# Kernel tuning notes

Hardware: AMD Instinct MI355X
Metric: run time of the kernel (lower is better)

Reference implementation:

```python
import jax, jax.numpy as jnp
import numpy as np

N = 100000
E = 1600000
IN_C, HID_C, OUT_C = 512, 128, 40
K = 5
ALPHA = 0.5


def setup_inputs() -> dict:
    key = jax.random.key(0)
    k1, k2, k3, k4, k5, k6 = jax.random.split(key, 6)
    x = jax.random.normal(k1, (N, IN_C), dtype=jnp.float32)
    edge_index = jax.random.randint(k2, (2, E), 0, N, dtype=jnp.int64)
    # lin1: in -> hidden, lin2: hidden -> out (Kaiming-uniform-ish scale)
    W1 = jax.random.normal(k3, (IN_C, HID_C), dtype=jnp.float32) * (1.0 / np.sqrt(IN_C))
    b1 = jax.random.normal(k4, (HID_C,), dtype=jnp.float32) * 0.01
    W2 = jax.random.normal(k5, (HID_C, OUT_C), dtype=jnp.float32) * (1.0 / np.sqrt(HID_C))
    b2 = jax.random.normal(k6, (OUT_C,), dtype=jnp.float32) * 0.01
    return {"x": x, "edge_index": edge_index, "W1": W1, "b1": b1, "W2": W2, "b2": b2}


def _gcn_norm(edge_index, num_nodes):
    # add self-loops with weight 1, then symmetric normalization D^-1/2 A D^-1/2
    loops = jnp.arange(num_nodes, dtype=edge_index.dtype)
    row = jnp.concatenate([edge_index[0], loops])
    col = jnp.concatenate([edge_index[1], loops])
    w = jnp.ones(row.shape[0], dtype=jnp.float32)
    deg = jax.ops.segment_sum(w, col, num_segments=num_nodes)
    dinv = jnp.where(deg > 0, jax.lax.rsqrt(deg), 0.0)
    norm = dinv[row] * w * dinv[col]
    return row, col, norm


def reference(x, edge_index, W1, b1, W2, b2):
    h = x @ W1 + b1                      # [N, HID_C]
    row, col, norm = _gcn_norm(edge_index, N)
    x0 = h
    for _ in range(K):
        # gather source features, scale by edge norm, scatter-add to targets
        agg = jax.ops.segment_sum(norm[:, None] * h[row], col, num_segments=N)
        h = (1.0 - ALPHA) * agg + ALPHA * x0
    return h @ W2 + b2                   # [N, OUT_C]
```

## Files before the change

### kernel.cpp

```cpp
#include <hip/hip_runtime.h>
#include <hip/hip_bf16.h>

#define NN 100000
#define EE 1600000
#define HALFN 50000

typedef __attribute__((ext_vector_type(8))) short short8;
typedef __attribute__((ext_vector_type(4))) float f32x4;

__device__ __forceinline__ unsigned short f2bfu(float f) {
    __hip_bfloat16 h = __float2bfloat16(f);
    return *reinterpret_cast<unsigned short*>(&h);
}
__device__ __forceinline__ float bf2f(unsigned short u) {
    return __uint_as_float((unsigned int)u << 16);
}


__global__ void wct_kernel(const float* __restrict__ W1, const float* __restrict__ W2,
                           const float* __restrict__ b1, short* __restrict__ WcT,
                           float* __restrict__ bc) {
    int t = blockIdx.x * 256 + threadIdx.x;
    if (t < 48 * 512) {
        int j = t >> 9, k = t & 511;
        float s = 0.f;
        if (j < 40)
            for (int i = 0; i < 128; ++i) s = fmaf(W1[k * 128 + i], W2[i * 40 + j], s);
        WcT[j * 512 + k] = (short)f2bfu(s);
    } else if (t < 48 * 512 + 48) {
        int j = t - 48 * 512;
        float s = 0.f;
        if (j < 40)
            for (int i = 0; i < 128; ++i) s = fmaf(b1[i], W2[i * 40 + j], s);
        bc[j] = s;
    }
}

__global__ __launch_bounds__(256) void gemm_z0(const float* __restrict__ x,
                                               const short* __restrict__ WcT,
                                               const float* __restrict__ bc,
                                               unsigned short* __restrict__ z0) {
    const int tid = threadIdx.x;
    const int lane = tid & 63;
    const int wave = tid >> 6;
    const int rbase = blockIdx.x * 64 + wave * 16;
    const int row = rbase + (lane & 15);
    const int kc = lane >> 4;
    const bool rok = row < NN;

    f32x4 acc0 = {0.f, 0.f, 0.f, 0.f};
    f32x4 acc1 = {0.f, 0.f, 0.f, 0.f};
    f32x4 acc2 = {0.f, 0.f, 0.f, 0.f};

    const float* xrow = x + (size_t)row * 512 + kc * 8;
    const short* bp0 = WcT + (size_t)(lane & 15) * 512 + kc * 8;
    const short* bp1 = bp0 + 16 * 512;
    const short* bp2 = bp0 + 32 * 512;

    for (int k0 = 0; k0 < 512; k0 += 32) {
        float4 p0 = {0.f, 0.f, 0.f, 0.f}, p1 = {0.f, 0.f, 0.f, 0.f};
        if (rok) {
            p0 = *reinterpret_cast<const float4*>(xrow + k0);
            p1 = *reinterpret_cast<const float4*>(xrow + k0 + 4);
        }
        short8 a;
        a[0] = (short)f2bfu(p0.x); a[1] = (short)f2bfu(p0.y);
        a[2] = (short)f2bfu(p0.z); a[3] = (short)f2bfu(p0.w);
        a[4] = (short)f2bfu(p1.x); a[5] = (short)f2bfu(p1.y);
        a[6] = (short)f2bfu(p1.z); a[7] = (short)f2bfu(p1.w);
        short8 b0 = *reinterpret_cast<const short8*>(bp0 + k0);
        short8 b1 = *reinterpret_cast<const short8*>(bp1 + k0);
        short8 b2 = *reinterpret_cast<const short8*>(bp2 + k0);
        acc0 = __builtin_amdgcn_mfma_f32_16x16x32_bf16(a, b0, acc0, 0, 0, 0);
        acc1 = __builtin_amdgcn_mfma_f32_16x16x32_bf16(a, b1, acc1, 0, 0, 0);
        acc2 = __builtin_amdgcn_mfma_f32_16x16x32_bf16(a, b2, acc2, 0, 0, 0);
    }

    const int cb = lane & 15;
    const int rr = rbase + (lane >> 4) * 4;
#pragma unroll
    for (int q = 0; q < 4; ++q) {
        int r = rr + q;
        if (r < NN) {
            z0[(size_t)r * 64 + cb] = f2bfu(acc0[q] + bc[cb]);
            z0[(size_t)r * 64 + cb + 16] = f2bfu(acc1[q] + bc[cb + 16]);
            z0[(size_t)r * 64 + cb + 32] = f2bfu(acc2[q] + bc[cb + 32]);
            z0[(size_t)r * 64 + cb + 48] = 0;
        }
    }
}

__global__ void count_kernel(const int* __restrict__ eidx, int* __restrict__ counts) {
    int e = blockIdx.x * 256 + threadIdx.x;
    if (e < EE) atomicAdd(&counts[eidx[EE + e]], 1);
}

__global__ void scan1(const int* __restrict__ counts, int* __restrict__ ptr,
                      int* __restrict__ bsum) {
    __shared__ int s[256];
    int tid = threadIdx.x;
    int i = blockIdx.x * 256 + tid;
    int v = (i < NN) ? counts[i] : 0;
    s[tid] = v;
    __syncthreads();
    for (int off = 1; off < 256; off <<= 1) {
        int t = (tid >= off) ? s[tid - off] : 0;
        __syncthreads();
        s[tid] += t;
        __syncthreads();
    }
    if (i < NN) ptr[i] = s[tid] - v;
    if (tid == 255) bsum[blockIdx.x] = s[255];
}

__global__ void scan2(int* __restrict__ bsum) {
    __shared__ int s[512];
    int tid = threadIdx.x;
    int v = (tid < 391) ? bsum[tid] : 0;
    s[tid] = v;
    __syncthreads();
    for (int off = 1; off < 512; off <<= 1) {
        int t = (tid >= off) ? s[tid - off] : 0;
        __syncthreads();
        s[tid] += t;
        __syncthreads();
    }
    if (tid < 391) bsum[tid] = s[tid] - v;
}

__global__ void scan3(int* __restrict__ ptr, const int* __restrict__ bsum,
                      const int* __restrict__ counts, float* __restrict__ dinvp,
                      int* __restrict__ ptr2) {
    int i = blockIdx.x * 256 + threadIdx.x;
    if (i < NN) {
        int p = ptr[i] + bsum[blockIdx.x];
        ptr[i] = p;
        ptr2[i] = p;
        dinvp[i] = rsqrtf(1.0f + (float)counts[i]);
    }
    if (i == 0) { ptr[NN] = EE; ptr2[NN] = EE; }
}

__global__ void scatter_kernel(const int* __restrict__ eidx,
                               const float* __restrict__ dinvp, int* __restrict__ ptr2,
                               int2* __restrict__ cev) {
    int e = blockIdx.x * 256 + threadIdx.x;
    if (e < EE) {
        int r = eidx[e];
        int c = eidx[EE + e];
        int pos = atomicAdd(&ptr2[c], 1);
        cev[pos] = make_int2(r, __float_as_int(dinvp[r]));
    }
}

__global__ __launch_bounds__(256, 8) void propagate(const unsigned short* __restrict__ zcur,
                                                    const unsigned short* __restrict__ z0q,
                                                    unsigned short* __restrict__ znb,
                                                    float* __restrict__ outf,
                                                    const int* __restrict__ ptr,
                                                    const int2* __restrict__ cev,
                                                    const float* __restrict__ dinvp,
                                                    const float* __restrict__ b2, int last) {
    const int lane = threadIdx.x & 63;
    const int wid = blockIdx.x * 4 + (threadIdx.x >> 6);
    const int n0 = wid, n1 = wid + HALFN;

    int beg0 = __builtin_amdgcn_readfirstlane(ptr[n0]);
    int end0 = __builtin_amdgcn_readfirstlane(ptr[n0 + 1]);
    int beg1 = __builtin_amdgcn_readfirstlane(ptr[n1]);
    int end1 = __builtin_amdgcn_readfirstlane(ptr[n1 + 1]);
    const float dc0 = dinvp[n0], dc1 = dinvp[n1];

    int m0 = end0 - beg0; if (m0 > 64) m0 = 64;
    int m1 = end1 - beg1; if (m1 > 64) m1 = 64;

    int idx0 = beg0 + (lane < m0 ? lane : m0 - 1); if (idx0 < 0) idx0 = 0;
    int idx1 = beg1 + (lane < m1 ? lane : m1 - 1); if (idx1 < 0) idx1 = 0;
    int2 ev0 = cev[idx0];
    int2 ev1 = cev[idx1];
    if (lane >= m0) ev0.y = 0;
    if (lane >= m1) ev1.y = 0;

    const float self0 = bf2f(zcur[(unsigned)(n0 * 64 + lane)]);
    const float self1 = bf2f(zcur[(unsigned)(n1 * 64 + lane)]);
    const float z00 = bf2f(z0q[(unsigned)(n0 * 64 + lane)]);
    const float z01 = bf2f(z0q[(unsigned)(n1 * 64 + lane)]);

    float A0 = dc0 * self0, B0 = 0.f;
    float A1 = dc1 * self1, B1 = 0.f;

    int nc0 = (m0 + 7) >> 3, nc1 = (m1 + 7) >> 3;
    int nc = nc0 > nc1 ? nc0 : nc1;
    for (int c = 0; c < nc; ++c) {
        const int j = c * 8;
        float x[8], y[8];
#pragma unroll
        for (int k = 0; k < 8; ++k) {
            unsigned r0 = (unsigned)__builtin_amdgcn_readlane(ev0.x, j + k);
            unsigned r1 = (unsigned)__builtin_amdgcn_readlane(ev1.x, j + k);
            x[k] = bf2f(zcur[(r0 << 6) + lane]);
            y[k] = bf2f(zcur[(r1 << 6) + lane]);
        }
#pragma unroll
        for (int k = 0; k < 8; ++k) {
            float w = __int_as_float(__builtin_amdgcn_readlane(ev0.y, j + k));
            float u = __int_as_float(__builtin_amdgcn_readlane(ev1.y, j + k));
            if (k & 1) { B0 = fmaf(w, x[k], B0); B1 = fmaf(u, y[k], B1); }
            else       { A0 = fmaf(w, x[k], A0); A1 = fmaf(u, y[k], A1); }
        }
    }

    for (int e = beg0 + 64; e < end0; ++e) {
        int2 ee = cev[e];
        A0 = fmaf(__int_as_float(ee.y), bf2f(zcur[((unsigned)ee.x << 6) + lane]), A0);
    }
    for (int e = beg1 + 64; e < end1; ++e) {
        int2 ee = cev[e];
        A1 = fmaf(__int_as_float(ee.y), bf2f(zcur[((unsigned)ee.x << 6) + lane]), A1);
    }

    float res0 = 0.5f * dc0 * (A0 + B0) + 0.5f * z00;
    float res1 = 0.5f * dc1 * (A1 + B1) + 0.5f * z01;
    if (last) {
        if (lane < 40) {
            outf[(unsigned)(n0 * 40 + lane)] = res0 + b2[lane];
            outf[(unsigned)(n1 * 40 + lane)] = res1 + b2[lane];
        }
    } else {
        znb[(unsigned)(n0 * 64 + lane)] = f2bfu(res0);
        znb[(unsigned)(n1 * 64 + lane)] = f2bfu(res1);
    }
}

extern "C" void kernel_launch(void* const* d_in, const int* in_sizes, int n_in,
                              void* d_out, int out_size, void* d_ws, size_t ws_size,
                              hipStream_t stream) {
    const float* x  = (const float*)d_in[0];
    const int*   ei = (const int*)d_in[1];
    const float* W1 = (const float*)d_in[2];
    const float* b1 = (const float*)d_in[3];
    const float* W2 = (const float*)d_in[4];
    const float* b2 = (const float*)d_in[5];
    float* out = (float*)d_out;

    char* ws = (char*)d_ws;
    short*          WcT  = (short*)(ws + 0);
    float*          bc   = (float*)(ws + 49152);
    unsigned short* z0   = (unsigned short*)(ws + 65536);
    unsigned short* za   = (unsigned short*)(ws + 12865536);
    unsigned short* zb   = (unsigned short*)(ws + 25665536);
    float*          dinv = (float*)(ws + 38465536);
    int*            cnt  = (int*)(ws + 38865536);
    int*            ptr  = (int*)(ws + 39265536);
    int*            bsum = (int*)(ws + 39665664);
    int*            ptr2 = (int*)(ws + 39667712);
    int2*           cev  = (int2*)(ws + 40067840);

    hipMemsetAsync(cnt, 0, NN * sizeof(int), stream);
    wct_kernel<<<97, 256, 0, stream>>>(W1, W2, b1, WcT, bc);
    count_kernel<<<(EE + 255) / 256, 256, 0, stream>>>(ei, cnt);
    scan1<<<391, 256, 0, stream>>>(cnt, ptr, bsum);
    scan2<<<1, 512, 0, stream>>>(bsum);
    scan3<<<391, 256, 0, stream>>>(ptr, bsum, cnt, dinv, ptr2);
    gemm_z0<<<1563, 256, 0, stream>>>(x, WcT, bc, z0);
    scatter_kernel<<<(EE + 255) / 256, 256, 0, stream>>>(ei, dinv, ptr2, cev);

    propagate<<<12500, 256, 0, stream>>>(z0, z0, zb, out, ptr, cev, dinv, b2, 0);
    propagate<<<12500, 256, 0, stream>>>(zb, z0, za, out, ptr, cev, dinv, b2, 0);
    propagate<<<12500, 256, 0, stream>>>(za, z0, zb, out, ptr, cev, dinv, b2, 0);
    propagate<<<12500, 256, 0, stream>>>(zb, z0, za, out, ptr, cev, dinv, b2, 0);
    propagate<<<12500, 256, 0, stream>>>(za, z0, zb, out, ptr, cev, dinv, b2, 1);
}
```

Measured before the change: 431.0 us.

## Split features into 16-channel planes and propagate each plane separately

```diff
diff --git a/kernel.cpp b/kernel.cpp
--- a/kernel.cpp
+++ b/kernel.cpp
@@ -3,7 +3,7 @@
 
 #define NN 100000
 #define EE 1600000
-#define HALFN 50000
+#define CH_STRIDE 1600000
 
 typedef __attribute__((ext_vector_type(8))) short short8;
 typedef __attribute__((ext_vector_type(4))) float f32x4;
@@ -82,10 +82,10 @@
     for (int q = 0; q < 4; ++q) {
         int r = rr + q;
         if (r < NN) {
-            z0[(size_t)r * 64 + cb] = f2bfu(acc0[q] + bc[cb]);
-            z0[(size_t)r * 64 + cb + 16] = f2bfu(acc1[q] + bc[cb + 16]);
-            z0[(size_t)r * 64 + cb + 32] = f2bfu(acc2[q] + bc[cb + 32]);
-            z0[(size_t)r * 64 + cb + 48] = 0;
+            unsigned ro = ((unsigned)r << 4) + cb;
+            z0[ro] = f2bfu(acc0[q] + bc[cb]);
+            z0[CH_STRIDE + ro] = f2bfu(acc1[q] + bc[cb + 16]);
+            z0[2 * CH_STRIDE + ro] = f2bfu(acc2[q] + bc[cb + 32]);
         }
     }
 }
@@ -153,82 +153,69 @@
     }
 }
 
-__global__ __launch_bounds__(256, 8) void propagate(const unsigned short* __restrict__ zcur,
-                                                    const unsigned short* __restrict__ z0q,
-                                                    unsigned short* __restrict__ znb,
-                                                    float* __restrict__ outf,
-                                                    const int* __restrict__ ptr,
-                                                    const int2* __restrict__ cev,
-                                                    const float* __restrict__ dinvp,
-                                                    const float* __restrict__ b2, int last) {
+__global__ __launch_bounds__(256) void propagate(const unsigned short* __restrict__ zcur,
+                                                 const unsigned short* __restrict__ z0q,
+                                                 unsigned short* __restrict__ znb,
+                                                 float* __restrict__ outf,
+                                                 const int* __restrict__ ptr,
+                                                 const int2* __restrict__ cev,
+                                                 const float* __restrict__ dinvp,
+                                                 const float* __restrict__ b2,
+                                                 int cid, int last) {
     const int lane = threadIdx.x & 63;
+    const int f = lane & 15;
+    const int g = lane >> 4;
     const int wid = blockIdx.x * 4 + (threadIdx.x >> 6);
-    const int n0 = wid, n1 = wid + HALFN;
-
-    int beg0 = __builtin_amdgcn_readfirstlane(ptr[n0]);
-    int end0 = __builtin_amdgcn_readfirstlane(ptr[n0 + 1]);
-    int beg1 = __builtin_amdgcn_readfirstlane(ptr[n1]);
-    int end1 = __builtin_amdgcn_readfirstlane(ptr[n1 + 1]);
-    const float dc0 = dinvp[n0], dc1 = dinvp[n1];
-
-    int m0 = end0 - beg0; if (m0 > 64) m0 = 64;
-    int m1 = end1 - beg1; if (m1 > 64) m1 = 64;
-
-    int idx0 = beg0 + (lane < m0 ? lane : m0 - 1); if (idx0 < 0) idx0 = 0;
-    int idx1 = beg1 + (lane < m1 ? lane : m1 - 1); if (idx1 < 0) idx1 = 0;
-    int2 ev0 = cev[idx0];
-    int2 ev1 = cev[idx1];
-    if (lane >= m0) ev0.y = 0;
-    if (lane >= m1) ev1.y = 0;
-
-    const float self0 = bf2f(zcur[(unsigned)(n0 * 64 + lane)]);
-    const float self1 = bf2f(zcur[(unsigned)(n1 * 64 + lane)]);
-    const float z00 = bf2f(z0q[(unsigned)(n0 * 64 + lane)]);
-    const float z01 = bf2f(z0q[(unsigned)(n1 * 64 + lane)]);
-
-    float A0 = dc0 * self0, B0 = 0.f;
-    float A1 = dc1 * self1, B1 = 0.f;
-
-    int nc0 = (m0 + 7) >> 3, nc1 = (m1 + 7) >> 3;
-    int nc = nc0 > nc1 ? nc0 : nc1;
-    for (int c = 0; c < nc; ++c) {
-        const int j = c * 8;
-        float x[8], y[8];
-#pragma unroll
-        for (int k = 0; k < 8; ++k) {
-            unsigned r0 = (unsigned)__builtin_amdgcn_readlane(ev0.x, j + k);
-            unsigned r1 = (unsigned)__builtin_amdgcn_readlane(ev1.x, j + k);
-            x[k] = bf2f(zcur[(r0 << 6) + lane]);
-            y[k] = bf2f(zcur[(r1 << 6) + lane]);
+    const int n = (wid << 2) + g;
+
+    const int beg = ptr[n];
+    const int deg = ptr[n + 1] - beg;
+    const float dc = dinvp[n];
+    const unsigned roff = ((unsigned)n << 4) + f;
+
+    float acc = dc * bf2f(zcur[roff]);
+    const float z0v = bf2f(z0q[roff]);
+
+    int maxd = deg;
+    maxd = max(maxd, __shfl_xor(maxd, 16, 64));
+    maxd = max(maxd, __shfl_xor(maxd, 32, 64));
+
+    for (int s = 0; s < maxd; s += 4) {
+        int i0, i1, i2, i3;
+        {
+            int t0 = (s + 0 < deg) ? s + 0 : deg - 1;
+            int t1 = (s + 1 < deg) ? s + 1 : deg - 1;
+            int t2 = (s + 2 < deg) ? s + 2 : deg - 1;
+            int t3 = (s + 3 < deg) ? s + 3 : deg - 1;
+            i0 = beg + t0; i0 = i0 < 0 ? 0 : (i0 >= EE ? EE - 1 : i0);
+            i1 = beg + t1; i1 = i1 < 0 ? 0 : (i1 >= EE ? EE - 1 : i1);
+            i2 = beg + t2; i2 = i2 < 0 ? 0 : (i2 >= EE ? EE - 1 : i2);
+            i3 = beg + t3; i3 = i3 < 0 ? 0 : (i3 >= EE ? EE - 1 : i3);
         }
-#pragma unroll
-        for (int k = 0; k < 8; ++k) {
-            float w = __int_as_float(__builtin_amdgcn_readlane(ev0.y, j + k));
-            float u = __int_as_float(__builtin_amdgcn_readlane(ev1.y, j + k));
-            if (k & 1) { B0 = fmaf(w, x[k], B0); B1 = fmaf(u, y[k], B1); }
-            else       { A0 = fmaf(w, x[k], A0); A1 = fmaf(u, y[k], A1); }
-        }
-    }
-
-    for (int e = beg0 + 64; e < end0; ++e) {
-        int2 ee = cev[e];
-        A0 = fmaf(__int_as_float(ee.y), bf2f(zcur[((unsigned)ee.x << 6) + lane]), A0);
-    }
-    for (int e = beg1 + 64; e < end1; ++e) {
-        int2 ee = cev[e];
-        A1 = fmaf(__int_as_float(ee.y), bf2f(zcur[((unsigned)ee.x << 6) + lane]), A1);
-    }
-
-    float res0 = 0.5f * dc0 * (A0 + B0) + 0.5f * z00;
-    float res1 = 0.5f * dc1 * (A1 + B1) + 0.5f * z01;
+        int2 e0 = cev[i0];
+        int2 e1 = cev[i1];
+        int2 e2 = cev[i2];
+        int2 e3 = cev[i3];
+        float x0 = bf2f(zcur[((unsigned)e0.x << 4) + f]);
+        float x1 = bf2f(zcur[((unsigned)e1.x << 4) + f]);
+        float x2 = bf2f(zcur[((unsigned)e2.x << 4) + f]);
+        float x3 = bf2f(zcur[((unsigned)e3.x << 4) + f]);
+        float w0 = (s + 0 < deg) ? __int_as_float(e0.y) : 0.f;
+        float w1 = (s + 1 < deg) ? __int_as_float(e1.y) : 0.f;
+        float w2 = (s + 2 < deg) ? __int_as_float(e2.y) : 0.f;
+        float w3 = (s + 3 < deg) ? __int_as_float(e3.y) : 0.f;
+        acc = fmaf(w0, x0, acc);
+        acc = fmaf(w1, x1, acc);
+        acc = fmaf(w2, x2, acc);
+        acc = fmaf(w3, x3, acc);
+    }
+
+    float res = 0.5f * dc * acc + 0.5f * z0v;
     if (last) {
-        if (lane < 40) {
-            outf[(unsigned)(n0 * 40 + lane)] = res0 + b2[lane];
-            outf[(unsigned)(n1 * 40 + lane)] = res1 + b2[lane];
-        }
+        int j = cid * 16 + f;
+        if (j < 40) outf[(unsigned)n * 40 + j] = res + b2[j];
     } else {
-        znb[(unsigned)(n0 * 64 + lane)] = f2bfu(res0);
-        znb[(unsigned)(n1 * 64 + lane)] = f2bfu(res1);
+        znb[roff] = f2bfu(res);
     }
 }
 
@@ -247,14 +234,14 @@
     short*          WcT  = (short*)(ws + 0);
     float*          bc   = (float*)(ws + 49152);
     unsigned short* z0   = (unsigned short*)(ws + 65536);
-    unsigned short* za   = (unsigned short*)(ws + 12865536);
-    unsigned short* zb   = (unsigned short*)(ws + 25665536);
-    float*          dinv = (float*)(ws + 38465536);
-    int*            cnt  = (int*)(ws + 38865536);
-    int*            ptr  = (int*)(ws + 39265536);
-    int*            bsum = (int*)(ws + 39665664);
-    int*            ptr2 = (int*)(ws + 39667712);
-    int2*           cev  = (int2*)(ws + 40067840);
+    unsigned short* za   = (unsigned short*)(ws + 9665536);
+    unsigned short* zb   = (unsigned short*)(ws + 19265536);
+    float*          dinv = (float*)(ws + 28865536);
+    int*            cnt  = (int*)(ws + 29265536);
+    int*            ptr  = (int*)(ws + 29665664);
+    int*            bsum = (int*)(ws + 30065792);
+    int*            ptr2 = (int*)(ws + 30067840);
+    int2*           cev  = (int2*)(ws + 30467968);
 
     hipMemsetAsync(cnt, 0, NN * sizeof(int), stream);
     wct_kernel<<<97, 256, 0, stream>>>(W1, W2, b1, WcT, bc);
@@ -265,9 +252,14 @@
     gemm_z0<<<1563, 256, 0, stream>>>(x, WcT, bc, z0);
     scatter_kernel<<<(EE + 255) / 256, 256, 0, stream>>>(ei, dinv, ptr2, cev);
 
-    propagate<<<12500, 256, 0, stream>>>(z0, z0, zb, out, ptr, cev, dinv, b2, 0);
-    propagate<<<12500, 256, 0, stream>>>(zb, z0, za, out, ptr, cev, dinv, b2, 0);
-    propagate<<<12500, 256, 0, stream>>>(za, z0, zb, out, ptr, cev, dinv, b2, 0);
-    propagate<<<12500, 256, 0, stream>>>(zb, z0, za, out, ptr, cev, dinv, b2, 0);
-    propagate<<<12500, 256, 0, stream>>>(za, z0, zb, out, ptr, cev, dinv, b2, 1);
-}
+    for (int c = 0; c < 3; ++c) {
+        const unsigned short* z0c = z0 + (size_t)c * CH_STRIDE;
+        unsigned short* zac = za + (size_t)c * CH_STRIDE;
+        unsigned short* zbc = zb + (size_t)c * CH_STRIDE;
+        propagate<<<6250, 256, 0, stream>>>(z0c, z0c, zbc, out, ptr, cev, dinv, b2, c, 0);
+        propagate<<<6250, 256, 0, stream>>>(zbc, z0c, zac, out, ptr, cev, dinv, b2, c, 0);
+        propagate<<<6250, 256, 0, stream>>>(zac, z0c, zbc, out, ptr, cev, dinv, b2, c, 0);
+        propagate<<<6250, 256, 0, stream>>>(zbc, z0c, zac, out, ptr, cev, dinv, b2, c, 0);
+        propagate<<<6250, 256, 0, stream>>>(zac, z0c, zbc, out, ptr, cev, dinv, b2, c, 1);
+    }
+}
```

Measured after the change: 639.3 us. 48.3% more time.

## Sort nodes by in-degree so each wave processes similarly sized node pairs

Applied to the files above, without the earlier changes.

```diff
diff --git a/kernel.cpp b/kernel.cpp
--- a/kernel.cpp
+++ b/kernel.cpp
@@ -3,7 +3,6 @@
 
 #define NN 100000
 #define EE 1600000
-#define HALFN 50000
 
 typedef __attribute__((ext_vector_type(8))) short short8;
 typedef __attribute__((ext_vector_type(4))) float f32x4;
@@ -141,6 +140,39 @@
     if (i == 0) { ptr[NN] = EE; ptr2[NN] = EE; }
 }
 
+__global__ void hist_kernel(const int* __restrict__ counts, int* __restrict__ hist) {
+    int i = blockIdx.x * 256 + threadIdx.x;
+    if (i < NN) {
+        int b = counts[i]; if (b > 255) b = 255;
+        atomicAdd(&hist[b], 1);
+    }
+}
+
+__global__ void hscan_kernel(int* __restrict__ hist) {
+    __shared__ int s[256];
+    int tid = threadIdx.x;
+    int v = hist[tid];
+    s[tid] = v;
+    __syncthreads();
+    for (int off = 1; off < 256; off <<= 1) {
+        int t = (tid >= off) ? s[tid - off] : 0;
+        __syncthreads();
+        s[tid] += t;
+        __syncthreads();
+    }
+    hist[tid] = s[tid] - v;
+}
+
+__global__ void place_kernel(const int* __restrict__ counts, int* __restrict__ hist,
+                             int* __restrict__ perm) {
+    int i = blockIdx.x * 256 + threadIdx.x;
+    if (i < NN) {
+        int b = counts[i]; if (b > 255) b = 255;
+        int pos = atomicAdd(&hist[b], 1);
+        perm[pos] = i;
+    }
+}
+
 __global__ void scatter_kernel(const int* __restrict__ eidx,
                                const float* __restrict__ dinvp, int* __restrict__ ptr2,
                                int2* __restrict__ cev) {
@@ -160,10 +192,12 @@
                                                     const int* __restrict__ ptr,
                                                     const int2* __restrict__ cev,
                                                     const float* __restrict__ dinvp,
-                                                    const float* __restrict__ b2, int last) {
+                                                    const float* __restrict__ b2,
+                                                    const int* __restrict__ perm, int last) {
     const int lane = threadIdx.x & 63;
     const int wid = blockIdx.x * 4 + (threadIdx.x >> 6);
-    const int n0 = wid, n1 = wid + HALFN;
+    const int n0 = __builtin_amdgcn_readfirstlane(perm[2 * wid]);
+    const int n1 = __builtin_amdgcn_readfirstlane(perm[2 * wid + 1]);
 
     int beg0 = __builtin_amdgcn_readfirstlane(ptr[n0]);
     int end0 = __builtin_amdgcn_readfirstlane(ptr[n0 + 1]);
@@ -255,19 +289,25 @@
     int*            bsum = (int*)(ws + 39665664);
     int*            ptr2 = (int*)(ws + 39667712);
     int2*           cev  = (int2*)(ws + 40067840);
+    int*            perm = (int*)(ws + 52867840);
+    int*            hist = (int*)(ws + 53267840);
 
     hipMemsetAsync(cnt, 0, NN * sizeof(int), stream);
+    hipMemsetAsync(hist, 0, 256 * sizeof(int), stream);
     wct_kernel<<<97, 256, 0, stream>>>(W1, W2, b1, WcT, bc);
     count_kernel<<<(EE + 255) / 256, 256, 0, stream>>>(ei, cnt);
     scan1<<<391, 256, 0, stream>>>(cnt, ptr, bsum);
     scan2<<<1, 512, 0, stream>>>(bsum);
     scan3<<<391, 256, 0, stream>>>(ptr, bsum, cnt, dinv, ptr2);
+    hist_kernel<<<391, 256, 0, stream>>>(cnt, hist);
+    hscan_kernel<<<1, 256, 0, stream>>>(hist);
+    place_kernel<<<391, 256, 0, stream>>>(cnt, hist, perm);
     gemm_z0<<<1563, 256, 0, stream>>>(x, WcT, bc, z0);
     scatter_kernel<<<(EE + 255) / 256, 256, 0, stream>>>(ei, dinv, ptr2, cev);
 
-    propagate<<<12500, 256, 0, stream>>>(z0, z0, zb, out, ptr, cev, dinv, b2, 0);
-    propagate<<<12500, 256, 0, stream>>>(zb, z0, za, out, ptr, cev, dinv, b2, 0);
-    propagate<<<12500, 256, 0, stream>>>(za, z0, zb, out, ptr, cev, dinv, b2, 0);
-    propagate<<<12500, 256, 0, stream>>>(zb, z0, za, out, ptr, cev, dinv, b2, 0);
-    propagate<<<12500, 256, 0, stream>>>(za, z0, zb, out, ptr, cev, dinv, b2, 1);
-}
+    propagate<<<12500, 256, 0, stream>>>(z0, z0, zb, out, ptr, cev, dinv, b2, perm, 0);
+    propagate<<<12500, 256, 0, stream>>>(zb, z0, za, out, ptr, cev, dinv, b2, perm, 0);
+    propagate<<<12500, 256, 0, stream>>>(za, z0, zb, out, ptr, cev, dinv, b2, perm, 0);
+    propagate<<<12500, 256, 0, stream>>>(zb, z0, za, out, ptr, cev, dinv, b2, perm, 0);
+    propagate<<<12500, 256, 0, stream>>>(za, z0, zb, out, ptr, cev, dinv, b2, perm, 1);
+}
```

Result: slower. 960.0 us (+122.8%).

## Propagate pre-scaled features y = dinv*z to drop per-edge weights

Applied to the files above, without the earlier changes.

```diff
diff --git a/kernel.cpp b/kernel.cpp
--- a/kernel.cpp
+++ b/kernel.cpp
@@ -36,10 +36,19 @@
     }
 }
 
+__global__ void padzero_kernel(unsigned short* __restrict__ ya,
+                               unsigned short* __restrict__ yb) {
+    int t = threadIdx.x;
+    if (t < 64) ya[(size_t)NN * 64 + t] = 0;
+    else if (t < 128) yb[(size_t)NN * 64 + (t - 64)] = 0;
+}
+
 __global__ __launch_bounds__(256) void gemm_z0(const float* __restrict__ x,
                                                const short* __restrict__ WcT,
                                                const float* __restrict__ bc,
-                                               unsigned short* __restrict__ z0) {
+                                               const float* __restrict__ dinvp,
+                                               unsigned short* __restrict__ z0,
+                                               unsigned short* __restrict__ y0) {
     const int tid = threadIdx.x;
     const int lane = tid & 63;
     const int wave = tid >> 6;
@@ -82,10 +91,18 @@
     for (int q = 0; q < 4; ++q) {
         int r = rr + q;
         if (r < NN) {
-            z0[(size_t)r * 64 + cb] = f2bfu(acc0[q] + bc[cb]);
-            z0[(size_t)r * 64 + cb + 16] = f2bfu(acc1[q] + bc[cb + 16]);
-            z0[(size_t)r * 64 + cb + 32] = f2bfu(acc2[q] + bc[cb + 32]);
+            float dc = dinvp[r];
+            float v0 = acc0[q] + bc[cb];
+            float v1 = acc1[q] + bc[cb + 16];
+            float v2 = acc2[q] + bc[cb + 32];
+            z0[(size_t)r * 64 + cb] = f2bfu(v0);
+            z0[(size_t)r * 64 + cb + 16] = f2bfu(v1);
+            z0[(size_t)r * 64 + cb + 32] = f2bfu(v2);
             z0[(size_t)r * 64 + cb + 48] = 0;
+            y0[(size_t)r * 64 + cb] = f2bfu(dc * v0);
+            y0[(size_t)r * 64 + cb + 16] = f2bfu(dc * v1);
+            y0[(size_t)r * 64 + cb + 32] = f2bfu(dc * v2);
+            y0[(size_t)r * 64 + cb + 48] = 0;
         }
     }
 }
@@ -141,24 +158,23 @@
     if (i == 0) { ptr[NN] = EE; ptr2[NN] = EE; }
 }
 
-__global__ void scatter_kernel(const int* __restrict__ eidx,
-                               const float* __restrict__ dinvp, int* __restrict__ ptr2,
-                               int2* __restrict__ cev) {
+__global__ void scatter_kernel(const int* __restrict__ eidx, int* __restrict__ ptr2,
+                               int* __restrict__ crow) {
     int e = blockIdx.x * 256 + threadIdx.x;
     if (e < EE) {
         int r = eidx[e];
         int c = eidx[EE + e];
         int pos = atomicAdd(&ptr2[c], 1);
-        cev[pos] = make_int2(r, __float_as_int(dinvp[r]));
-    }
-}
-
-__global__ __launch_bounds__(256, 8) void propagate(const unsigned short* __restrict__ zcur,
+        crow[pos] = r;
+    }
+}
+
+__global__ __launch_bounds__(256, 8) void propagate(const unsigned short* __restrict__ ycur,
                                                     const unsigned short* __restrict__ z0q,
-                                                    unsigned short* __restrict__ znb,
+                                                    unsigned short* __restrict__ ynb,
                                                     float* __restrict__ outf,
                                                     const int* __restrict__ ptr,
-                                                    const int2* __restrict__ cev,
+                                                    const int* __restrict__ crow,
                                                     const float* __restrict__ dinvp,
                                                     const float* __restrict__ b2, int last) {
     const int lane = threadIdx.x & 63;
@@ -176,18 +192,15 @@
 
     int idx0 = beg0 + (lane < m0 ? lane : m0 - 1); if (idx0 < 0) idx0 = 0;
     int idx1 = beg1 + (lane < m1 ? lane : m1 - 1); if (idx1 < 0) idx1 = 0;
-    int2 ev0 = cev[idx0];
-    int2 ev1 = cev[idx1];
-    if (lane >= m0) ev0.y = 0;
-    if (lane >= m1) ev1.y = 0;
-
-    const float self0 = bf2f(zcur[(unsigned)(n0 * 64 + lane)]);
-    const float self1 = bf2f(zcur[(unsigned)(n1 * 64 + lane)]);
+    int r0v = crow[idx0];
+    int r1v = crow[idx1];
+    if (lane >= m0) r0v = NN;
+    if (lane >= m1) r1v = NN;
+
+    float A0 = bf2f(ycur[(unsigned)(n0 * 64 + lane)]), B0 = 0.f;
+    float A1 = bf2f(ycur[(unsigned)(n1 * 64 + lane)]), B1 = 0.f;
     const float z00 = bf2f(z0q[(unsigned)(n0 * 64 + lane)]);
     const float z01 = bf2f(z0q[(unsigned)(n1 * 64 + lane)]);
-
-    float A0 = dc0 * self0, B0 = 0.f;
-    float A1 = dc1 * self1, B1 = 0.f;
 
     int nc0 = (m0 + 7) >> 3, nc1 = (m1 + 7) >> 3;
     int nc = nc0 > nc1 ? nc0 : nc1;
@@ -196,39 +209,33 @@
         float x[8], y[8];
 #pragma unroll
         for (int k = 0; k < 8; ++k) {
-            unsigned r0 = (unsigned)__builtin_amdgcn_readlane(ev0.x, j + k);
-            unsigned r1 = (unsigned)__builtin_amdgcn_readlane(ev1.x, j + k);
-            x[k] = bf2f(zcur[(r0 << 6) + lane]);
-            y[k] = bf2f(zcur[(r1 << 6) + lane]);
+            unsigned r0 = (unsigned)__builtin_amdgcn_readlane(r0v, j + k);
+            unsigned r1 = (unsigned)__builtin_amdgcn_readlane(r1v, j + k);
+            x[k] = bf2f(ycur[(r0 << 6) + lane]);
+            y[k] = bf2f(ycur[(r1 << 6) + lane]);
         }
 #pragma unroll
         for (int k = 0; k < 8; ++k) {
-            float w = __int_as_float(__builtin_amdgcn_readlane(ev0.y, j + k));
-            float u = __int_as_float(__builtin_amdgcn_readlane(ev1.y, j + k));
-            if (k & 1) { B0 = fmaf(w, x[k], B0); B1 = fmaf(u, y[k], B1); }
-            else       { A0 = fmaf(w, x[k], A0); A1 = fmaf(u, y[k], A1); }
-        }
-    }
-
-    for (int e = beg0 + 64; e < end0; ++e) {
-        int2 ee = cev[e];
-        A0 = fmaf(__int_as_float(ee.y), bf2f(zcur[((unsigned)ee.x << 6) + lane]), A0);
-    }
-    for (int e = beg1 + 64; e < end1; ++e) {
-        int2 ee = cev[e];
-        A1 = fmaf(__int_as_float(ee.y), bf2f(zcur[((unsigned)ee.x << 6) + lane]), A1);
-    }
-
-    float res0 = 0.5f * dc0 * (A0 + B0) + 0.5f * z00;
-    float res1 = 0.5f * dc1 * (A1 + B1) + 0.5f * z01;
+            if (k & 1) { B0 += x[k]; B1 += y[k]; }
+            else       { A0 += x[k]; A1 += y[k]; }
+        }
+    }
+
+    for (int e = beg0 + 64; e < end0; ++e)
+        A0 += bf2f(ycur[((unsigned)crow[e] << 6) + lane]);
+    for (int e = beg1 + 64; e < end1; ++e)
+        A1 += bf2f(ycur[((unsigned)crow[e] << 6) + lane]);
+
+    float rz0 = fmaf(0.5f * dc0, A0 + B0, 0.5f * z00);
+    float rz1 = fmaf(0.5f * dc1, A1 + B1, 0.5f * z01);
     if (last) {
         if (lane < 40) {
-            outf[(unsigned)(n0 * 40 + lane)] = res0 + b2[lane];
-            outf[(unsigned)(n1 * 40 + lane)] = res1 + b2[lane];
+            outf[(unsigned)(n0 * 40 + lane)] = rz0 + b2[lane];
+            outf[(unsigned)(n1 * 40 + lane)] = rz1 + b2[lane];
         }
     } else {
-        znb[(unsigned)(n0 * 64 + lane)] = f2bfu(res0);
-        znb[(unsigned)(n1 * 64 + lane)] = f2bfu(res1);
+        ynb[(unsigned)(n0 * 64 + lane)] = f2bfu(dc0 * rz0);
+        ynb[(unsigned)(n1 * 64 + lane)] = f2bfu(dc1 * rz1);
     }
 }
 
@@ -247,27 +254,28 @@
     short*          WcT  = (short*)(ws + 0);
     float*          bc   = (float*)(ws + 49152);
     unsigned short* z0   = (unsigned short*)(ws + 65536);
-    unsigned short* za   = (unsigned short*)(ws + 12865536);
-    unsigned short* zb   = (unsigned short*)(ws + 25665536);
-    float*          dinv = (float*)(ws + 38465536);
-    int*            cnt  = (int*)(ws + 38865536);
-    int*            ptr  = (int*)(ws + 39265536);
-    int*            bsum = (int*)(ws + 39665664);
-    int*            ptr2 = (int*)(ws + 39667712);
-    int2*           cev  = (int2*)(ws + 40067840);
+    unsigned short* ya   = (unsigned short*)(ws + 12865536);
+    unsigned short* yb   = (unsigned short*)(ws + 25678592);
+    float*          dinv = (float*)(ws + 38491648);
+    int*            cnt  = (int*)(ws + 38891648);
+    int*            ptr  = (int*)(ws + 39291648);
+    int*            bsum = (int*)(ws + 39691776);
+    int*            ptr2 = (int*)(ws + 39693824);
+    int*            crow = (int*)(ws + 40093952);
 
     hipMemsetAsync(cnt, 0, NN * sizeof(int), stream);
     wct_kernel<<<97, 256, 0, stream>>>(W1, W2, b1, WcT, bc);
+    padzero_kernel<<<1, 128, 0, stream>>>(ya, yb);
     count_kernel<<<(EE + 255) / 256, 256, 0, stream>>>(ei, cnt);
     scan1<<<391, 256, 0, stream>>>(cnt, ptr, bsum);
     scan2<<<1, 512, 0, stream>>>(bsum);
     scan3<<<391, 256, 0, stream>>>(ptr, bsum, cnt, dinv, ptr2);
-    gemm_z0<<<1563, 256, 0, stream>>>(x, WcT, bc, z0);
-    scatter_kernel<<<(EE + 255) / 256, 256, 0, stream>>>(ei, dinv, ptr2, cev);
-
-    propagate<<<12500, 256, 0, stream>>>(z0, z0, zb, out, ptr, cev, dinv, b2, 0);
-    propagate<<<12500, 256, 0, stream>>>(zb, z0, za, out, ptr, cev, dinv, b2, 0);
-    propagate<<<12500, 256, 0, stream>>>(za, z0, zb, out, ptr, cev, dinv, b2, 0);
-    propagate<<<12500, 256, 0, stream>>>(zb, z0, za, out, ptr, cev, dinv, b2, 0);
-    propagate<<<12500, 256, 0, stream>>>(za, z0, zb, out, ptr, cev, dinv, b2, 1);
-}
+    gemm_z0<<<1563, 256, 0, stream>>>(x, WcT, bc, dinv, z0, ya);
+    scatter_kernel<<<(EE + 255) / 256, 256, 0, stream>>>(ei, ptr2, crow);
+
+    propagate<<<12500, 256, 0, stream>>>(ya, z0, yb, out, ptr, crow, dinv, b2, 0);
+    propagate<<<12500, 256, 0, stream>>>(yb, z0, ya, out, ptr, crow, dinv, b2, 0);
+    propagate<<<12500, 256, 0, stream>>>(ya, z0, yb, out, ptr, crow, dinv, b2, 0);
+    propagate<<<12500, 256, 0, stream>>>(yb, z0, ya, out, ptr, crow, dinv, b2, 0);
+    propagate<<<12500, 256, 0, stream>>>(ya, z0, yb, out, ptr, crow, dinv, b2, 1);
+}
```

Measured after the change: 446.9 us. 1.04x slower.
